# Kernel tuning notes

Measured on AMD Instinct MI355X. Metric: run time of the kernel, lower is better.

## Reference

```python
import jax, jax.numpy as jnp
import numpy as np

N, DQ, T, H1 = 131072, 256, 4, 512

def setup_inputs() -> dict:
    key = jax.random.key(0)
    k_q, k_w0, k_b0, k_w1, k_z = jax.random.split(key, 5)
    return {
        "q": jax.random.normal(k_q, (N, DQ), dtype=jnp.float32),
        "Z": jax.random.randint(k_z, (N,), 0, T, dtype=jnp.int32),
        "W0": jax.random.normal(k_w0, (T, DQ, H1), dtype=jnp.float32) * (1.0 / np.sqrt(DQ)),
        "b0": jax.random.normal(k_b0, (T, H1), dtype=jnp.float32) * 0.01,
        "W1": jax.random.normal(k_w1, (T, H1), dtype=jnp.float32) * (1.0 / np.sqrt(H1)),
        "b1": jnp.zeros((), dtype=jnp.float32),
    }

def reference(q, Z, W0, b0, W1, b1):
    # Dense grouped-GEMM over all T types (T is small), then select per-atom
    # type result. Avoids materializing the per-atom [N, dq, h1] gathered
    # weight tensor that tf.gather would create.
    h_all = jnp.einsum('nd,tdh->nth', q, W0)              # [N, T, H1]
    h = jnp.take_along_axis(h_all, Z[:, None, None].astype(jnp.int32), axis=1)[:, 0, :]  # [N, H1]
    h = jnp.tanh(h + b0[Z])                               # hidden activations
    F = jnp.einsum('nh,nh->n', h, W1[Z]) + b1             # [N]
    return F
```

## Files before the change

### kernel.cpp

```cpp
#include <hip/hip_runtime.h>
#include <hip/hip_bf16.h>

#define N_ATOMS 131072
#define DQ 256
#define H1 512
#define NTYPES 4
#define TILE_M 64
#define GRID 1024

typedef __bf16 bf16x8 __attribute__((ext_vector_type(8)));
typedef float f32x16 __attribute__((ext_vector_type(16)));

__device__ __forceinline__ unsigned short f2bf(float f) {
  unsigned int u = __builtin_bit_cast(unsigned int, f);
  u += 0x7fffu + ((u >> 16) & 1u);
  return (unsigned short)(u >> 16);
}

__device__ __forceinline__ float fast_tanh(float x) {
  float e = __expf(2.0f * x);
  return 1.0f - 2.0f * __builtin_amdgcn_rcpf(e + 1.0f);
}

__global__ __launch_bounds__(64) void init_kernel(int* __restrict__ hdr) {
  if (threadIdx.x < 16) hdr[threadIdx.x] = 0;
}

__global__ __launch_bounds__(256) void prep_kernel(
    const float* __restrict__ W0, const int* __restrict__ Z,
    unsigned short* __restrict__ W0s, int* __restrict__ perm,
    int* __restrict__ cnt)
{
  const int b = blockIdx.x, tid = threadIdx.x;
  const int gid = b * 256 + tid;

  if (gid < NTYPES * (DQ / 8) * H1) {
    const int n  = gid & (H1 - 1);
    const int kg = (gid >> 9) & 31;
    const int t  = gid >> 14;
    const float* src = W0 + ((size_t)(t * DQ + kg * 8) * H1 + n);
    unsigned short o[8];
#pragma unroll
    for (int j = 0; j < 8; ++j) o[j] = f2bf(src[(size_t)j * H1]);
    uint4 v;
    v.x = (unsigned)o[0] | ((unsigned)o[1] << 16);
    v.y = (unsigned)o[2] | ((unsigned)o[3] << 16);
    v.z = (unsigned)o[4] | ((unsigned)o[5] << 16);
    v.w = (unsigned)o[6] | ((unsigned)o[7] << 16);
    ((uint4*)W0s)[gid] = v;
  }

  __shared__ int lc[NTYPES], lbase[NTYPES];
  if (tid < NTYPES) lc[tid] = 0;
  __syncthreads();
  const int t  = Z[gid];
  const int my = atomicAdd(&lc[t], 1);
  __syncthreads();
  if (tid < NTYPES) lbase[tid] = lc[tid] ? atomicAdd(&cnt[tid], lc[tid]) : 0;
  __syncthreads();
  perm[t * N_ATOMS + lbase[t] + my] = gid;
}

__device__ __forceinline__ void issue_half(float4* st, const float* q,
                                           int atom, int c4, int h) {
  const float* p = q + (size_t)atom * DQ + c4 * 64 + h * 32;
#pragma unroll
  for (int i = 0; i < 8; ++i) st[i] = *(const float4*)(p + i * 4);
}

__device__ __forceinline__ void store_half(
    const float4* st, unsigned short (*A)[TILE_M][8], int row, int c4, int h) {
#pragma unroll
  for (int i2 = 0; i2 < 4; ++i2) {
    const int k = c4 * 64 + h * 32 + i2 * 8;
    uint4 vv;
    vv.x = (unsigned)f2bf(st[2*i2].x)   | ((unsigned)f2bf(st[2*i2].y)   << 16);
    vv.y = (unsigned)f2bf(st[2*i2].z)   | ((unsigned)f2bf(st[2*i2].w)   << 16);
    vv.z = (unsigned)f2bf(st[2*i2+1].x) | ((unsigned)f2bf(st[2*i2+1].y) << 16);
    vv.w = (unsigned)f2bf(st[2*i2+1].z) | ((unsigned)f2bf(st[2*i2+1].w) << 16);
    *(uint4*)&A[k >> 3][row][0] = vv;
  }
}

__global__ __launch_bounds__(256, 2) void gemm_persist(
    const float* __restrict__ q, const int* __restrict__ perm,
    const int* __restrict__ cnt, int* __restrict__ ticket,
    const unsigned short* __restrict__ W0s,
    const float* __restrict__ b0g, const float* __restrict__ W1,
    const float* __restrict__ b1p, float* __restrict__ out)
{
  __shared__ unsigned short Alds[2][DQ / 8][TILE_M][8];
  __shared__ float Fws[2][4][TILE_M];
  __shared__ int shvt[2];

  const int tid = threadIdx.x;
  const int l = tid & 63, w = tid >> 6;
  const int half = l >> 5, ln = l & 31;
  const int row = tid >> 2, c4 = tid & 3;

  const int c0 = cnt[0], c1 = cnt[1], c2 = cnt[2], c3 = cnt[3];
  const int n0 = (c0 + 63) >> 6, n1 = (c1 + 63) >> 6;
  const int n2 = (c2 + 63) >> 6, n3 = (c3 + 63) >> 6;
  const int p1 = n0, p2 = n0 + n1, p3 = n0 + n1 + n2;
  const int total = n0 + n1 + n2 + n3;
  const float b1v = b1p[0];

#define DECODE(v, T, J0, CT) do {                                   \
    T = ((v) >= p1) + ((v) >= p2) + ((v) >= p3);                    \
    const int pre_ = (T == 0) ? 0 : (T == 1) ? p1 : (T == 2) ? p2 : p3; \
    CT = (T == 0) ? c0 : (T == 1) ? c1 : (T == 2) ? c2 : c3;        \
    J0 = ((v) - pre_) * TILE_M; } while (0)

#define EPI_HALF(MT) do {                                                     \
    _Pragma("unroll")                                                         \
    for (int r = 0; r < 16; ++r) {                                            \
      float s = 0.f;                                                          \
      _Pragma("unroll")                                                       \
      for (int nt = 0; nt < 4; ++nt)                                          \
        s += w1v[nt] * fast_tanh(acc[MT][nt][r] + b0v[nt]);                   \
      s += __shfl_xor(s, 1);                                                  \
      s += __shfl_xor(s, 2);                                                  \
      s += __shfl_xor(s, 4);                                                  \
      s += __shfl_xor(s, 8);                                                  \
      s += __shfl_xor(s, 16);                                                 \
      if (ln == 0)                                                            \
        Fws[cur][w][(MT) * 32 + (r & 3) + 8 * (r >> 2) + 4 * half] = s;       \
    }                                                                         \
  } while (0)

  int vt_cur = (int)blockIdx.x;
  int t_cur, j0_cur, ct_cur;
  DECODE(vt_cur, t_cur, j0_cur, ct_cur);

  float4 st[8];
  {
    int atom = 0;
    if (j0_cur + row < ct_cur) atom = perm[t_cur * N_ATOMS + j0_cur + row];
    issue_half(st, q, atom, c4, 0);
    store_half(st, Alds[0], row, c4, 0);
    issue_half(st, q, atom, c4, 1);
    store_half(st, Alds[0], row, c4, 1);
  }
  if (tid == 0) shvt[0] = GRID + atomicAdd(ticket, 1);
  __syncthreads();

  int vt_nxt = shvt[0];
  int t_nxt = 0, j0_nxt = 0, ct_nxt = 0, anext = 0;
  if (vt_nxt < total) {
    DECODE(vt_nxt, t_nxt, j0_nxt, ct_nxt);
    if (j0_nxt + row < ct_nxt) anext = perm[t_nxt * N_ATOMS + j0_nxt + row];
  }
  int cur = 0, par = 0;

  while (vt_cur < total) {
    f32x16 acc[2][4];
#pragma unroll
    for (int mt = 0; mt < 2; ++mt)
#pragma unroll
      for (int nt = 0; nt < 4; ++nt) acc[mt][nt] = (f32x16)0.0f;

    const unsigned short* Bt = W0s + (size_t)t_cur * (DQ * H1);
    const unsigned short* Bbase = Bt + (size_t)(w * 128 + ln) * 8;

    __builtin_amdgcn_s_setprio(1);
#pragma unroll 4
    for (int step = 0; step < 16; ++step) {
      const int kg = 2 * step + half;
      const bf16x8 a0 = *(const bf16x8*)&Alds[cur][kg][ln][0];
      const bf16x8 a1 = *(const bf16x8*)&Alds[cur][kg][32 + ln][0];
      const unsigned short* bp = Bbase + (size_t)kg * (H1 * 8);
      const bf16x8 b0f = *(const bf16x8*)(bp);
      const bf16x8 b1f = *(const bf16x8*)(bp + 32 * 8);
      const bf16x8 b2f = *(const bf16x8*)(bp + 64 * 8);
      const bf16x8 b3f = *(const bf16x8*)(bp + 96 * 8);
      acc[0][0] = __builtin_amdgcn_mfma_f32_32x32x16_bf16(a0, b0f, acc[0][0], 0, 0, 0);
      acc[1][0] = __builtin_amdgcn_mfma_f32_32x32x16_bf16(a1, b0f, acc[1][0], 0, 0, 0);
      acc[0][1] = __builtin_amdgcn_mfma_f32_32x32x16_bf16(a0, b1f, acc[0][1], 0, 0, 0);
      acc[1][1] = __builtin_amdgcn_mfma_f32_32x32x16_bf16(a1, b1f, acc[1][1], 0, 0, 0);
      acc[0][2] = __builtin_amdgcn_mfma_f32_32x32x16_bf16(a0, b2f, acc[0][2], 0, 0, 0);
      acc[1][2] = __builtin_amdgcn_mfma_f32_32x32x16_bf16(a1, b2f, acc[1][2], 0, 0, 0);
      acc[0][3] = __builtin_amdgcn_mfma_f32_32x32x16_bf16(a0, b3f, acc[0][3], 0, 0, 0);
      acc[1][3] = __builtin_amdgcn_mfma_f32_32x32x16_bf16(a1, b3f, acc[1][3], 0, 0, 0);
    }
    __builtin_amdgcn_s_setprio(0);

    const bool have_nxt = (vt_nxt < total);

    float b0v[4], w1v[4];
#pragma unroll
    for (int nt = 0; nt < 4; ++nt) {
      const int c = w * 128 + nt * 32 + ln;
      b0v[nt] = b0g[t_cur * H1 + c];
      w1v[nt] = W1[t_cur * H1 + c];
    }

    if (have_nxt) issue_half(st, q, anext, c4, 0);
    EPI_HALF(0);
    if (have_nxt) store_half(st, Alds[cur ^ 1], row, c4, 0);

    if (have_nxt) issue_half(st, q, anext, c4, 1);
    EPI_HALF(1);
    if (have_nxt) store_half(st, Alds[cur ^ 1], row, c4, 1);

    if (tid == 0 && have_nxt) shvt[par ^ 1] = GRID + atomicAdd(ticket, 1);

    __syncthreads();

    if (tid < TILE_M && j0_cur + tid < ct_cur) {
      const int a = perm[t_cur * N_ATOMS + j0_cur + tid];
      out[a] = Fws[cur][0][tid] + Fws[cur][1][tid] + Fws[cur][2][tid]
             + Fws[cur][3][tid] + b1v;
    }

    if (have_nxt) {
      vt_cur = vt_nxt; t_cur = t_nxt; j0_cur = j0_nxt; ct_cur = ct_nxt;
      vt_nxt = shvt[par ^ 1];
      anext = 0;
      if (vt_nxt < total) {
        DECODE(vt_nxt, t_nxt, j0_nxt, ct_nxt);
        if (j0_nxt + row < ct_nxt) anext = perm[t_nxt * N_ATOMS + j0_nxt + row];
      }
    } else {
      vt_cur = total;
    }
    cur ^= 1; par ^= 1;
  }
#undef DECODE
#undef EPI_HALF
}

extern "C" void kernel_launch(void* const* d_in, const int* in_sizes, int n_in,
                              void* d_out, int out_size, void* d_ws, size_t ws_size,
                              hipStream_t stream) {
  const float* q  = (const float*)d_in[0];
  const int*   Z  = (const int*)d_in[1];
  const float* W0 = (const float*)d_in[2];
  const float* b0 = (const float*)d_in[3];
  const float* W1 = (const float*)d_in[4];
  const float* b1 = (const float*)d_in[5];
  float* out = (float*)d_out;

  char* ws = (char*)d_ws;
  int* hdr    = (int*)(ws);
  int* cnt    = hdr;
  int* ticket = hdr + 4;
  int* perm   = (int*)(ws + 64);
  unsigned short* W0s =
      (unsigned short*)(ws + 64 + (size_t)NTYPES * N_ATOMS * 4);

  hipLaunchKernelGGL(init_kernel, dim3(1), dim3(64), 0, stream, hdr);
  hipLaunchKernelGGL(prep_kernel, dim3(512), dim3(256), 0, stream,
                     W0, Z, W0s, perm, cnt);
  hipLaunchKernelGGL(gemm_persist, dim3(GRID), dim3(256), 0, stream,
                     q, perm, cnt, ticket, W0s, b0, W1, b1, out);
}
```

Measured before the change: 279.5 us.

## Replace atomic ticket scheduler with static grid-stride tiles and staggered K order

```diff
diff --git a/kernel.cpp b/kernel.cpp
--- a/kernel.cpp
+++ b/kernel.cpp
@@ -6,7 +6,7 @@
 #define H1 512
 #define NTYPES 4
 #define TILE_M 64
-#define GRID 1024
+#define GRID 512
 
 typedef __bf16 bf16x8 __attribute__((ext_vector_type(8)));
 typedef float f32x16 __attribute__((ext_vector_type(16)));
@@ -84,19 +84,20 @@
 
 __global__ __launch_bounds__(256, 2) void gemm_persist(
     const float* __restrict__ q, const int* __restrict__ perm,
-    const int* __restrict__ cnt, int* __restrict__ ticket,
+    const int* __restrict__ cnt,
     const unsigned short* __restrict__ W0s,
     const float* __restrict__ b0g, const float* __restrict__ W1,
     const float* __restrict__ b1p, float* __restrict__ out)
 {
   __shared__ unsigned short Alds[2][DQ / 8][TILE_M][8];
   __shared__ float Fws[2][4][TILE_M];
-  __shared__ int shvt[2];
 
   const int tid = threadIdx.x;
   const int l = tid & 63, w = tid >> 6;
   const int half = l >> 5, ln = l & 31;
   const int row = tid >> 2, c4 = tid & 3;
+  const int bx = (int)blockIdx.x;
+  const int kphase = bx & 15;
 
   const int c0 = cnt[0], c1 = cnt[1], c2 = cnt[2], c3 = cnt[3];
   const int n0 = (c0 + 63) >> 6, n1 = (c1 + 63) >> 6;
@@ -128,7 +129,7 @@
     }                                                                         \
   } while (0)
 
-  int vt_cur = (int)blockIdx.x;
+  int vt_cur = bx;
   int t_cur, j0_cur, ct_cur;
   DECODE(vt_cur, t_cur, j0_cur, ct_cur);
 
@@ -141,16 +142,15 @@
     issue_half(st, q, atom, c4, 1);
     store_half(st, Alds[0], row, c4, 1);
   }
-  if (tid == 0) shvt[0] = GRID + atomicAdd(ticket, 1);
-  __syncthreads();
-
-  int vt_nxt = shvt[0];
+  __syncthreads();
+
+  int vt_nxt = bx + GRID;
   int t_nxt = 0, j0_nxt = 0, ct_nxt = 0, anext = 0;
   if (vt_nxt < total) {
     DECODE(vt_nxt, t_nxt, j0_nxt, ct_nxt);
     if (j0_nxt + row < ct_nxt) anext = perm[t_nxt * N_ATOMS + j0_nxt + row];
   }
-  int cur = 0, par = 0;
+  int cur = 0;
 
   while (vt_cur < total) {
     f32x16 acc[2][4];
@@ -165,14 +165,14 @@
     __builtin_amdgcn_s_setprio(1);
 #pragma unroll 4
     for (int step = 0; step < 16; ++step) {
-      const int kg = 2 * step + half;
+      const int kg = 2 * ((step + kphase) & 15) + half;
       const bf16x8 a0 = *(const bf16x8*)&Alds[cur][kg][ln][0];
       const bf16x8 a1 = *(const bf16x8*)&Alds[cur][kg][32 + ln][0];
-      const unsigned short* bp = Bbase + (size_t)kg * (H1 * 8);
-      const bf16x8 b0f = *(const bf16x8*)(bp);
-      const bf16x8 b1f = *(const bf16x8*)(bp + 32 * 8);
-      const bf16x8 b2f = *(const bf16x8*)(bp + 64 * 8);
-      const bf16x8 b3f = *(const bf16x8*)(bp + 96 * 8);
+      const unsigned short* bptr = Bbase + (size_t)kg * (H1 * 8);
+      const bf16x8 b0f = *(const bf16x8*)(bptr);
+      const bf16x8 b1f = *(const bf16x8*)(bptr + 32 * 8);
+      const bf16x8 b2f = *(const bf16x8*)(bptr + 64 * 8);
+      const bf16x8 b3f = *(const bf16x8*)(bptr + 96 * 8);
       acc[0][0] = __builtin_amdgcn_mfma_f32_32x32x16_bf16(a0, b0f, acc[0][0], 0, 0, 0);
       acc[1][0] = __builtin_amdgcn_mfma_f32_32x32x16_bf16(a1, b0f, acc[1][0], 0, 0, 0);
       acc[0][1] = __builtin_amdgcn_mfma_f32_32x32x16_bf16(a0, b1f, acc[0][1], 0, 0, 0);
@@ -202,8 +202,6 @@
     EPI_HALF(1);
     if (have_nxt) store_half(st, Alds[cur ^ 1], row, c4, 1);
 
-    if (tid == 0 && have_nxt) shvt[par ^ 1] = GRID + atomicAdd(ticket, 1);
-
     __syncthreads();
 
     if (tid < TILE_M && j0_cur + tid < ct_cur) {
@@ -212,18 +210,17 @@
              + Fws[cur][3][tid] + b1v;
     }
 
+    vt_cur = vt_nxt;
     if (have_nxt) {
-      vt_cur = vt_nxt; t_cur = t_nxt; j0_cur = j0_nxt; ct_cur = ct_nxt;
-      vt_nxt = shvt[par ^ 1];
+      t_cur = t_nxt; j0_cur = j0_nxt; ct_cur = ct_nxt;
+      vt_nxt += GRID;
       anext = 0;
       if (vt_nxt < total) {
         DECODE(vt_nxt, t_nxt, j0_nxt, ct_nxt);
         if (j0_nxt + row < ct_nxt) anext = perm[t_nxt * N_ATOMS + j0_nxt + row];
       }
-    } else {
-      vt_cur = total;
-    }
-    cur ^= 1; par ^= 1;
+    }
+    cur ^= 1;
   }
 #undef DECODE
 #undef EPI_HALF
@@ -243,7 +240,6 @@
   char* ws = (char*)d_ws;
   int* hdr    = (int*)(ws);
   int* cnt    = hdr;
-  int* ticket = hdr + 4;
   int* perm   = (int*)(ws + 64);
   unsigned short* W0s =
       (unsigned short*)(ws + 64 + (size_t)NTYPES * N_ATOMS * 4);
@@ -252,5 +248,5 @@
   hipLaunchKernelGGL(prep_kernel, dim3(512), dim3(256), 0, stream,
                      W0, Z, W0s, perm, cnt);
   hipLaunchKernelGGL(gemm_persist, dim3(GRID), dim3(256), 0, stream,
-                     q, perm, cnt, ticket, W0s, b0, W1, b1, out);
-}
+                     q, perm, cnt, W0s, b0, W1, b1, out);
+}
```

Result: faster. 271.8 us (-2.8%).
